# Performance work log

Measured on AMD Instinct MI355X. Metric: run time of the kernel, lower is better.

## Reference

```python
import jax, jax.numpy as jnp
import numpy as np

DIM = 256
H = 4
D = DIM // H  # head_dim = 64
SCALE = D ** -0.5


def setup_inputs() -> dict:
    key = jax.random.key(0)
    ks = jax.random.split(key, 12)
    B, N, M = 4, 2048, 2048
    x_query = jax.random.normal(ks[0], (B, N, DIM), dtype=jnp.float32)
    x_context = jax.random.normal(ks[1], (B, M, DIM), dtype=jnp.float32)
    geo_bias = jax.random.normal(ks[2], (B, H, N, M), dtype=jnp.float32)
    init = 1.0 / np.sqrt(DIM)
    Wq = jax.random.uniform(ks[3], (DIM, DIM), jnp.float32, -init, init)
    bq = jax.random.uniform(ks[4], (DIM,), jnp.float32, -init, init)
    Wk = jax.random.uniform(ks[5], (DIM, DIM), jnp.float32, -init, init)
    bk = jax.random.uniform(ks[6], (DIM,), jnp.float32, -init, init)
    Wv = jax.random.uniform(ks[7], (DIM, DIM), jnp.float32, -init, init)
    bv = jax.random.uniform(ks[8], (DIM,), jnp.float32, -init, init)
    Wo = jax.random.uniform(ks[9], (DIM, DIM), jnp.float32, -init, init)
    bo = jax.random.uniform(ks[10], (DIM,), jnp.float32, -init, init)
    return {"x_query": x_query, "x_context": x_context, "geo_bias": geo_bias,
            "Wq": Wq, "bq": bq, "Wk": Wk, "bk": bk, "Wv": Wv, "bv": bv,
            "Wo": Wo, "bo": bo}


def reference(x_query, x_context, geo_bias, Wq, bq, Wk, bk, Wv, bv, Wo, bo):
    B, N, _ = x_query.shape
    M = x_context.shape[1]
    # projections; nn.Linear computes x @ W.T + b
    q = (x_query @ Wq.T + bq).reshape(B, N, H, D).transpose(0, 2, 1, 3)   # (B,H,N,D)
    k = (x_context @ Wk.T + bk).reshape(B, M, H, D).transpose(0, 2, 1, 3)  # (B,H,M,D)
    v = (x_context @ Wv.T + bv).reshape(B, M, H, D).transpose(0, 2, 1, 3)  # (B,H,M,D)
    attn = jnp.einsum("bhnd,bhmd->bhnm", q, k) * SCALE + geo_bias
    attn = jax.nn.softmax(attn, axis=-1)
    out = jnp.einsum("bhnm,bhmd->bhnd", attn, v)
    out = out.transpose(0, 2, 1, 3).reshape(B, N, DIM)
    return out @ Wo.T + bo
```

## Files before the change

### kernel.cpp

```cpp
#include <hip/hip_runtime.h>

typedef unsigned short u16;
typedef unsigned int u32;
using bf16x8  = __attribute__((ext_vector_type(8))) __bf16;
using u16x8   = __attribute__((ext_vector_type(8), may_alias)) u16;
using u16x4   = __attribute__((ext_vector_type(4), may_alias)) u16;
using f32x4   = __attribute__((ext_vector_type(4))) float;
using f32x4_a = __attribute__((ext_vector_type(4), may_alias)) float;

#define DEV __device__ __forceinline__

constexpr int Bn = 4, Hn = 4, Nn = 2048, Mn = 2048, Dn = 64, DIMn = 256;
constexpr float SCALEc = 0.125f;
constexpr float SHIFTc = 12.0f;
constexpr int LSTRIDE = 152;

DEV float bf2f(u16 h) { u32 u = ((u32)h) << 16; return __builtin_bit_cast(float, u); }
DEV u16 f2bf(float f) {
    u32 u = __builtin_bit_cast(u32, f);
    u += 0x7fffu + ((u >> 16) & 1u);
    return (u16)(u >> 16);
}
DEV bf16x8 ld8bf(const u16* p) {
    return __builtin_bit_cast(bf16x8, *reinterpret_cast<const u16x8*>(p));
}
DEV bf16x8 ld8f_bf(const float* p) {
    const f32x4 a = *reinterpret_cast<const f32x4_a*>(p);
    const f32x4 b = *reinterpret_cast<const f32x4_a*>(p + 4);
    u16x8 r;
    r[0] = f2bf(a[0]); r[1] = f2bf(a[1]); r[2] = f2bf(a[2]); r[3] = f2bf(a[3]);
    r[4] = f2bf(b[0]); r[5] = f2bf(b[1]); r[6] = f2bf(b[2]); r[7] = f2bf(b[3]);
    return __builtin_bit_cast(bf16x8, r);
}

__global__ __launch_bounds__(256, 4) void qkv_kernel(
    const float* __restrict__ Xq, const float* __restrict__ Wq, const float* __restrict__ bq,
    const float* __restrict__ Xc, const float* __restrict__ Wk, const float* __restrict__ bk,
    const float* __restrict__ Wv, const float* __restrict__ bv,
    float* __restrict__ Q, u16* __restrict__ K, u16* __restrict__ V)
{
    const int wave = threadIdx.x >> 6, lane = threadIdx.x & 63;
    const int quad = lane >> 4, l16 = lane & 15;
    const int o0 = wave * 64;

    if (blockIdx.x < 512) {
        const int row0 = blockIdx.x * 16;
        const int b = row0 >> 11, n0 = row0 & 2047;
        f32x4 acc[4] = {};
        #pragma unroll
        for (int k0 = 0; k0 < 256; k0 += 32) {
            bf16x8 wf[4];
            const bf16x8 af = ld8f_bf(Xq + (size_t)(row0 + l16) * DIMn + k0 + quad * 8);
            #pragma unroll
            for (int os = 0; os < 4; os++)
                wf[os] = ld8f_bf(Wq + (size_t)(o0 + os * 16 + l16) * DIMn + k0 + quad * 8);
            #pragma unroll
            for (int os = 0; os < 4; os++)
                acc[os] = __builtin_amdgcn_mfma_f32_16x16x32_bf16(af, wf[os], acc[os], 0, 0, 0);
        }
        #pragma unroll
        for (int os = 0; os < 4; os++) {
            const int col = o0 + os * 16 + l16;
            const int h = col >> 6, d = col & 63;
            const float bb = bq[col];
            #pragma unroll
            for (int r = 0; r < 4; r++) {
                const int n = n0 + quad * 4 + r;
                Q[((size_t)(b * Hn + h) * Nn + n) * Dn + d] = acc[os][r] + bb;
            }
        }
    } else {
        const int row0 = (blockIdx.x - 512) * 16;
        const int b = row0 >> 11, n0 = row0 & 2047;
        f32x4 ack[4] = {};
        f32x4 acv[4] = {};
        #pragma unroll
        for (int k0 = 0; k0 < 256; k0 += 32) {
            bf16x8 wkf[4], wvf[4];
            const bf16x8 af = ld8f_bf(Xc + (size_t)(row0 + l16) * DIMn + k0 + quad * 8);
            #pragma unroll
            for (int os = 0; os < 4; os++) {
                wkf[os] = ld8f_bf(Wk + (size_t)(o0 + os * 16 + l16) * DIMn + k0 + quad * 8);
                wvf[os] = ld8f_bf(Wv + (size_t)(o0 + os * 16 + l16) * DIMn + k0 + quad * 8);
            }
            #pragma unroll
            for (int os = 0; os < 4; os++) {
                ack[os] = __builtin_amdgcn_mfma_f32_16x16x32_bf16(af, wkf[os], ack[os], 0, 0, 0);
                acv[os] = __builtin_amdgcn_mfma_f32_16x16x32_bf16(wvf[os], af, acv[os], 0, 0, 0);
            }
        }
        #pragma unroll
        for (int os = 0; os < 4; os++) {
            const int col = o0 + os * 16 + l16;
            const int h = col >> 6, d = col & 63;
            const float bb = bk[col];
            #pragma unroll
            for (int r = 0; r < 4; r++) {
                const int m = n0 + quad * 4 + r;
                K[((size_t)(b * Hn + h) * Mn + m) * Dn + d] = f2bf(ack[os][r] + bb);
            }
        }
        #pragma unroll
        for (int os = 0; os < 4; os++)
            #pragma unroll
            for (int r = 0; r < 4; r++) {
                const int colf = o0 + os * 16 + quad * 4 + r;
                const int h = colf >> 6, d = colf & 63;
                const float bb = bv[colf];
                const int m = n0 + l16;
                V[((size_t)(b * Hn + h) * Dn + d) * Mn + m] = f2bf(acv[os][r] + bb);
            }
    }
}

__global__ __launch_bounds__(256, 4) void attn_kernel(
    const float* __restrict__ Q,
    const u16* __restrict__ K,
    const u16* __restrict__ V,
    const float* __restrict__ geo,
    float* __restrict__ Pnum,
    float* __restrict__ Lsum,
    int S)
{
    __shared__ __align__(16) u16 lds[4][16 * LSTRIDE];

    const int h = blockIdx.y;
    const int b = blockIdx.z / S, split = blockIdx.z % S;
    const int wave = threadIdx.x >> 6, lane = threadIdx.x & 63;
    const int quad = lane >> 4, l16 = lane & 15;
    const int nbase = blockIdx.x * 64 + wave * 16;
    const int mlen = Mn / S, mbeg = split * mlen, mend = mbeg + mlen;

    const float* Qh = Q + ((size_t)(b * Hn + h) * Nn + nbase) * Dn;
    const u16*   Kh = K + (size_t)(b * Hn + h) * Mn * Dn;
    const u16*   Vh = V + (size_t)(b * Hn + h) * Dn * Mn;
    const float* Gl = geo + ((size_t)(b * Hn + h) * Nn + nbase + l16) * (size_t)Mn + quad * 4;

    bf16x8 qh[2], ql[2];
    #pragma unroll
    for (int kh = 0; kh < 2; kh++) {
        const float* qp = Qh + (size_t)l16 * Dn + kh * 32 + quad * 8;
        const f32x4 a = *reinterpret_cast<const f32x4_a*>(qp);
        const f32x4 c = *reinterpret_cast<const f32x4_a*>(qp + 4);
        u16x8 hi, lo;
        #pragma unroll
        for (int j = 0; j < 4; j++) {
            hi[j] = f2bf(a[j]); lo[j] = f2bf(a[j] - bf2f(hi[j]));
            hi[4 + j] = f2bf(c[j]); lo[4 + j] = f2bf(c[j] - bf2f(hi[4 + j]));
        }
        qh[kh] = __builtin_bit_cast(bf16x8, hi);
        ql[kh] = __builtin_bit_cast(bf16x8, lo);
    }

    f32x4 oacc[4] = {};
    float lsum = 0.f;
    u16* pl = &lds[wave][0];
    const u16* kbase = Kh + (size_t)l16 * Dn + quad * 8;
    const u16* vbase = Vh + (size_t)l16 * Mn + quad * 8;

    f32x4 g[8];
    #pragma unroll
    for (int ms = 0; ms < 8; ms++)
        g[ms] = *reinterpret_cast<const f32x4_a*>(Gl + mbeg + ms * 16);
    bf16x8 kb0 = ld8bf(kbase + (size_t)mbeg * Dn);
    bf16x8 kb1 = ld8bf(kbase + (size_t)mbeg * Dn + 32);

    for (int m0 = mbeg; m0 < mend; m0 += 128) {
        #pragma unroll
        for (int ms = 0; ms < 8; ms++) {
            int mb = m0 + (ms + 1) * 16;
            if (mb > mend - 16) mb = mend - 16;
            const u16* kp = kbase + (size_t)mb * Dn;
            const bf16x8 nk0 = ld8bf(kp);
            const bf16x8 nk1 = ld8bf(kp + 32);
            f32x4 s = {};
            __builtin_amdgcn_s_setprio(1);
            s = __builtin_amdgcn_mfma_f32_16x16x32_bf16(kb0, qh[0], s, 0, 0, 0);
            s = __builtin_amdgcn_mfma_f32_16x16x32_bf16(kb0, ql[0], s, 0, 0, 0);
            s = __builtin_amdgcn_mfma_f32_16x16x32_bf16(kb1, qh[1], s, 0, 0, 0);
            s = __builtin_amdgcn_mfma_f32_16x16x32_bf16(kb1, ql[1], s, 0, 0, 0);
            __builtin_amdgcn_s_setprio(0);
            u16x4 pk;
            float ls = 0.f;
            #pragma unroll
            for (int r = 0; r < 4; r++) {
                const float p = __expf(fmaf(s[r], SCALEc, g[ms][r]) - SHIFTc);
                ls += p;
                pk[r] = f2bf(p);
            }
            lsum += ls;
            *reinterpret_cast<u16x4*>(pl + l16 * LSTRIDE + ms * 16 + quad * 4) = pk;
            kb0 = nk0; kb1 = nk1;
        }
        if (m0 + 128 < mend) {
            #pragma unroll
            for (int ms = 0; ms < 8; ms++)
                g[ms] = *reinterpret_cast<const f32x4_a*>(Gl + m0 + 128 + ms * 16);
        }
        #pragma unroll
        for (int kh = 0; kh < 4; kh++) {
            const bf16x8 pa = ld8bf(pl + l16 * LSTRIDE + kh * 32 + quad * 8);
            bf16x8 vb[4];
            #pragma unroll
            for (int ds = 0; ds < 4; ds++)
                vb[ds] = ld8bf(vbase + (size_t)(ds * 16) * Mn + m0 + kh * 32);
            __builtin_amdgcn_s_setprio(1);
            #pragma unroll
            for (int ds = 0; ds < 4; ds++)
                oacc[ds] = __builtin_amdgcn_mfma_f32_16x16x32_bf16(pa, vb[ds], oacc[ds], 0, 0, 0);
            __builtin_amdgcn_s_setprio(0);
        }
    }

    lsum += __shfl_xor(lsum, 16);
    lsum += __shfl_xor(lsum, 32);

    float* PN = Pnum + (size_t)split * (Bn * (size_t)Nn * DIMn)
                     + ((size_t)b * Nn + nbase) * DIMn + h * Dn;
    #pragma unroll
    for (int r = 0; r < 4; r++)
        #pragma unroll
        for (int ds = 0; ds < 4; ds++)
            PN[(size_t)(quad * 4 + r) * DIMn + ds * 16 + l16] = oacc[ds][r];

    if (lane < 16)
        Lsum[(((size_t)split * Bn + b) * Hn + h) * Nn + nbase + l16] = lsum;
}

__global__ __launch_bounds__(256, 4) void oproj_kernel(
    const float* __restrict__ Pnum, const float* __restrict__ Lsum,
    const float* __restrict__ W, const float* __restrict__ bias,
    float* __restrict__ out, int S)
{
    const int row0 = blockIdx.x * 16;
    const int wave = threadIdx.x >> 6, lane = threadIdx.x & 63;
    const int quad = lane >> 4, l16 = lane & 15;
    const int o0 = wave * 64;
    const size_t slab = (size_t)Bn * Nn * DIMn;

    const int arow = row0 + l16;
    const int b = arow >> 11, n = arow & 2047;
    float inv[4];
    #pragma unroll
    for (int hh = 0; hh < 4; hh++) {
        float l = 0.f;
        for (int s = 0; s < S; s++)
            l += Lsum[(((size_t)s * Bn + b) * Hn + hh) * Nn + n];
        inv[hh] = 1.0f / l;
    }

    f32x4 acc[4] = {};
    #pragma unroll
    for (int k0 = 0; k0 < 256; k0 += 32) {
        bf16x8 wf[4];
        #pragma unroll
        for (int os = 0; os < 4; os++)
            wf[os] = ld8f_bf(W + (size_t)(o0 + os * 16 + l16) * DIMn + k0 + quad * 8);
        f32x4 a0 = {}, a1 = {};
        for (int s = 0; s < S; s++) {
            const float* p = Pnum + (size_t)s * slab + (size_t)arow * DIMn + k0 + quad * 8;
            a0 += *reinterpret_cast<const f32x4_a*>(p);
            a1 += *reinterpret_cast<const f32x4_a*>(p + 4);
        }
        const float iv = inv[(k0 + quad * 8) >> 6];
        u16x8 r;
        #pragma unroll
        for (int j = 0; j < 4; j++) {
            r[j]     = f2bf(a0[j] * iv);
            r[4 + j] = f2bf(a1[j] * iv);
        }
        const bf16x8 af = __builtin_bit_cast(bf16x8, r);
        #pragma unroll
        for (int os = 0; os < 4; os++)
            acc[os] = __builtin_amdgcn_mfma_f32_16x16x32_bf16(af, wf[os], acc[os], 0, 0, 0);
    }
    #pragma unroll
    for (int os = 0; os < 4; os++) {
        const int col = o0 + os * 16 + l16;
        const float bb = bias[col];
        #pragma unroll
        for (int r = 0; r < 4; r++) {
            const int row = row0 + quad * 4 + r;
            out[(size_t)row * DIMn + col] = acc[os][r] + bb;
        }
    }
}

extern "C" void kernel_launch(void* const* d_in, const int* in_sizes, int n_in,
                              void* d_out, int out_size, void* d_ws, size_t ws_size,
                              hipStream_t stream) {
    const float* xq  = (const float*)d_in[0];
    const float* xc  = (const float*)d_in[1];
    const float* geo = (const float*)d_in[2];
    const float* Wq  = (const float*)d_in[3];
    const float* bq  = (const float*)d_in[4];
    const float* Wk  = (const float*)d_in[5];
    const float* bk  = (const float*)d_in[6];
    const float* Wv  = (const float*)d_in[7];
    const float* bv  = (const float*)d_in[8];
    const float* Wo  = (const float*)d_in[9];
    const float* bo  = (const float*)d_in[10];

    const int S = (ws_size >= (60ull << 20)) ? 4 : 1;

    char* ws = (char*)d_ws;
    float* Qw   = (float*)ws;
    u16*   Kw   = (u16*)(ws + (8ull << 20));
    u16*   Vw   = (u16*)(ws + (12ull << 20));
    float* Pnum = (float*)(ws + (20ull << 20));
    float* Lsum = (float*)(ws + (20ull << 20) + (size_t)S * (8ull << 20));

    qkv_kernel<<<1024, 256, 0, stream>>>(xq, Wq, bq, xc, Wk, bk, Wv, bv, Qw, Kw, Vw);
    attn_kernel<<<dim3(Nn / 64, Hn, Bn * S), 256, 0, stream>>>(Qw, Kw, Vw, geo, Pnum, Lsum, S);
    oproj_kernel<<<Bn * Nn / 16, 256, 0, stream>>>(Pnum, Lsum, Wo, bo, (float*)d_out, S);
}
```

Baseline: 561.3 us.

## Stream geo_bias into LDS via direct global-to-LDS loads and prefetch V fragments

The attention kernel now fetches geo_bias tiles with global_load_lds straight into a per-wave LDS buffer instead of holding them in registers, with explicit waitcnt fences around the refill. The V fragments used in the PV matmul are software-pipelined one step ahead. Launch-bound occupancy hints are dropped and weight loads in the projection kernels are interleaved with MFMAs. The aim is to cut register pressure and hide the latency of the large geo_bias stream, at the cost of more LDS use per block, which can limit occupancy, and coarse vmcnt(0) waits.

```diff
diff --git a/kernel.cpp b/kernel.cpp
--- a/kernel.cpp
+++ b/kernel.cpp
@@ -33,7 +33,13 @@
     return __builtin_bit_cast(bf16x8, r);
 }
 
-__global__ __launch_bounds__(256, 4) void qkv_kernel(
+typedef __attribute__((address_space(1))) const unsigned int as1_uint;
+typedef __attribute__((address_space(3))) unsigned int as3_uint;
+DEV void dma16(const float* g, float* l) {
+    __builtin_amdgcn_global_load_lds((as1_uint*)g, (as3_uint*)l, 16, 0, 0);
+}
+
+__global__ __launch_bounds__(256) void qkv_kernel(
     const float* __restrict__ Xq, const float* __restrict__ Wq, const float* __restrict__ bq,
     const float* __restrict__ Xc, const float* __restrict__ Wk, const float* __restrict__ bk,
     const float* __restrict__ Wv, const float* __restrict__ bv,
@@ -49,14 +55,12 @@
         f32x4 acc[4] = {};
         #pragma unroll
         for (int k0 = 0; k0 < 256; k0 += 32) {
-            bf16x8 wf[4];
             const bf16x8 af = ld8f_bf(Xq + (size_t)(row0 + l16) * DIMn + k0 + quad * 8);
             #pragma unroll
-            for (int os = 0; os < 4; os++)
-                wf[os] = ld8f_bf(Wq + (size_t)(o0 + os * 16 + l16) * DIMn + k0 + quad * 8);
-            #pragma unroll
-            for (int os = 0; os < 4; os++)
-                acc[os] = __builtin_amdgcn_mfma_f32_16x16x32_bf16(af, wf[os], acc[os], 0, 0, 0);
+            for (int os = 0; os < 4; os++) {
+                const bf16x8 wf = ld8f_bf(Wq + (size_t)(o0 + os * 16 + l16) * DIMn + k0 + quad * 8);
+                acc[os] = __builtin_amdgcn_mfma_f32_16x16x32_bf16(af, wf, acc[os], 0, 0, 0);
+            }
         }
         #pragma unroll
         for (int os = 0; os < 4; os++) {
@@ -76,17 +80,13 @@
         f32x4 acv[4] = {};
         #pragma unroll
         for (int k0 = 0; k0 < 256; k0 += 32) {
-            bf16x8 wkf[4], wvf[4];
             const bf16x8 af = ld8f_bf(Xc + (size_t)(row0 + l16) * DIMn + k0 + quad * 8);
             #pragma unroll
             for (int os = 0; os < 4; os++) {
-                wkf[os] = ld8f_bf(Wk + (size_t)(o0 + os * 16 + l16) * DIMn + k0 + quad * 8);
-                wvf[os] = ld8f_bf(Wv + (size_t)(o0 + os * 16 + l16) * DIMn + k0 + quad * 8);
-            }
-            #pragma unroll
-            for (int os = 0; os < 4; os++) {
-                ack[os] = __builtin_amdgcn_mfma_f32_16x16x32_bf16(af, wkf[os], ack[os], 0, 0, 0);
-                acv[os] = __builtin_amdgcn_mfma_f32_16x16x32_bf16(wvf[os], af, acv[os], 0, 0, 0);
+                const bf16x8 wkf = ld8f_bf(Wk + (size_t)(o0 + os * 16 + l16) * DIMn + k0 + quad * 8);
+                ack[os] = __builtin_amdgcn_mfma_f32_16x16x32_bf16(af, wkf, ack[os], 0, 0, 0);
+                const bf16x8 wvf = ld8f_bf(Wv + (size_t)(o0 + os * 16 + l16) * DIMn + k0 + quad * 8);
+                acv[os] = __builtin_amdgcn_mfma_f32_16x16x32_bf16(wvf, af, acv[os], 0, 0, 0);
             }
         }
         #pragma unroll
@@ -113,7 +113,7 @@
     }
 }
 
-__global__ __launch_bounds__(256, 4) void attn_kernel(
+__global__ __launch_bounds__(256) void attn_kernel(
     const float* __restrict__ Q,
     const u16* __restrict__ K,
     const u16* __restrict__ V,
@@ -122,7 +122,8 @@
     float* __restrict__ Lsum,
     int S)
 {
-    __shared__ __align__(16) u16 lds[4][16 * LSTRIDE];
+    __shared__ __align__(16) u16 plds[4][16 * LSTRIDE];
+    __shared__ __align__(16) float glds[4][8][256];
 
     const int h = blockIdx.y;
     const int b = blockIdx.z / S, split = blockIdx.z % S;
@@ -154,18 +155,20 @@
 
     f32x4 oacc[4] = {};
     float lsum = 0.f;
-    u16* pl = &lds[wave][0];
+    u16* pl = &plds[wave][0];
+    float* gw = &glds[wave][0][0];
+    const float* gr = gw + lane * 4;
     const u16* kbase = Kh + (size_t)l16 * Dn + quad * 8;
     const u16* vbase = Vh + (size_t)l16 * Mn + quad * 8;
 
-    f32x4 g[8];
     #pragma unroll
     for (int ms = 0; ms < 8; ms++)
-        g[ms] = *reinterpret_cast<const f32x4_a*>(Gl + mbeg + ms * 16);
+        dma16(Gl + mbeg + ms * 16, gw + ms * 256);
     bf16x8 kb0 = ld8bf(kbase + (size_t)mbeg * Dn);
     bf16x8 kb1 = ld8bf(kbase + (size_t)mbeg * Dn + 32);
 
     for (int m0 = mbeg; m0 < mend; m0 += 128) {
+        asm volatile("s_waitcnt vmcnt(0)" ::: "memory");
         #pragma unroll
         for (int ms = 0; ms < 8; ms++) {
             int mb = m0 + (ms + 1) * 16;
@@ -180,11 +183,12 @@
             s = __builtin_amdgcn_mfma_f32_16x16x32_bf16(kb1, qh[1], s, 0, 0, 0);
             s = __builtin_amdgcn_mfma_f32_16x16x32_bf16(kb1, ql[1], s, 0, 0, 0);
             __builtin_amdgcn_s_setprio(0);
+            const f32x4 g = *reinterpret_cast<const f32x4_a*>(gr + ms * 256);
             u16x4 pk;
             float ls = 0.f;
             #pragma unroll
             for (int r = 0; r < 4; r++) {
-                const float p = __expf(fmaf(s[r], SCALEc, g[ms][r]) - SHIFTc);
+                const float p = __expf(fmaf(s[r], SCALEc, g[r]) - SHIFTc);
                 ls += p;
                 pk[r] = f2bf(p);
             }
@@ -193,22 +197,30 @@
             kb0 = nk0; kb1 = nk1;
         }
         if (m0 + 128 < mend) {
+            asm volatile("s_waitcnt lgkmcnt(0)" ::: "memory");
             #pragma unroll
             for (int ms = 0; ms < 8; ms++)
-                g[ms] = *reinterpret_cast<const f32x4_a*>(Gl + m0 + 128 + ms * 16);
-        }
+                dma16(Gl + (m0 + 128) + ms * 16, gw + ms * 256);
+        }
+        bf16x8 vcur[4], vnxt[4];
+        #pragma unroll
+        for (int ds = 0; ds < 4; ds++)
+            vcur[ds] = ld8bf(vbase + (size_t)(ds * 16) * Mn + m0);
         #pragma unroll
         for (int kh = 0; kh < 4; kh++) {
+            if (kh < 3) {
+                #pragma unroll
+                for (int ds = 0; ds < 4; ds++)
+                    vnxt[ds] = ld8bf(vbase + (size_t)(ds * 16) * Mn + m0 + (kh + 1) * 32);
+            }
             const bf16x8 pa = ld8bf(pl + l16 * LSTRIDE + kh * 32 + quad * 8);
-            bf16x8 vb[4];
+            __builtin_amdgcn_s_setprio(1);
             #pragma unroll
             for (int ds = 0; ds < 4; ds++)
-                vb[ds] = ld8bf(vbase + (size_t)(ds * 16) * Mn + m0 + kh * 32);
-            __builtin_amdgcn_s_setprio(1);
-            #pragma unroll
-            for (int ds = 0; ds < 4; ds++)
-                oacc[ds] = __builtin_amdgcn_mfma_f32_16x16x32_bf16(pa, vb[ds], oacc[ds], 0, 0, 0);
+                oacc[ds] = __builtin_amdgcn_mfma_f32_16x16x32_bf16(pa, vcur[ds], oacc[ds], 0, 0, 0);
             __builtin_amdgcn_s_setprio(0);
+            #pragma unroll
+            for (int ds = 0; ds < 4; ds++) vcur[ds] = vnxt[ds];
         }
     }
 
@@ -227,7 +239,7 @@
         Lsum[(((size_t)split * Bn + b) * Hn + h) * Nn + nbase + l16] = lsum;
 }
 
-__global__ __launch_bounds__(256, 4) void oproj_kernel(
+__global__ __launch_bounds__(256) void oproj_kernel(
     const float* __restrict__ Pnum, const float* __restrict__ Lsum,
     const float* __restrict__ W, const float* __restrict__ bias,
     float* __restrict__ out, int S)
@@ -252,10 +264,6 @@
     f32x4 acc[4] = {};
     #pragma unroll
     for (int k0 = 0; k0 < 256; k0 += 32) {
-        bf16x8 wf[4];
-        #pragma unroll
-        for (int os = 0; os < 4; os++)
-            wf[os] = ld8f_bf(W + (size_t)(o0 + os * 16 + l16) * DIMn + k0 + quad * 8);
         f32x4 a0 = {}, a1 = {};
         for (int s = 0; s < S; s++) {
             const float* p = Pnum + (size_t)s * slab + (size_t)arow * DIMn + k0 + quad * 8;
@@ -271,8 +279,10 @@
         }
         const bf16x8 af = __builtin_bit_cast(bf16x8, r);
         #pragma unroll
-        for (int os = 0; os < 4; os++)
-            acc[os] = __builtin_amdgcn_mfma_f32_16x16x32_bf16(af, wf[os], acc[os], 0, 0, 0);
+        for (int os = 0; os < 4; os++) {
+            const bf16x8 wf = ld8f_bf(W + (size_t)(o0 + os * 16 + l16) * DIMn + k0 + quad * 8);
+            acc[os] = __builtin_amdgcn_mfma_f32_16x16x32_bf16(af, wf, acc[os], 0, 0, 0);
+        }
     }
     #pragma unroll
     for (int os = 0; os < 4; os++) {
```

Result: no change. 553.8 us (-1.3%).
